# Kernel tuning notes

Measured on AMD Instinct MI355X. Metric: run time of the kernel, lower is better.

## Reference

```python
import jax, jax.numpy as jnp
import numpy as np

# ---- grid / solver constants (from opt) ----
NZ, NX = 300, 400
NPML, NPAD = 32, 0
NZP = NZ + 2 * NPML + NPAD   # 364 padded depth
NXP = NX + 2 * NPML          # 464 padded width
NSTEPS = 200
NSHOTS = 2
DX = 0.01    # km (moduli scaled by 1e-6 => velocities in km/s)
DT = 0.001   # s
SRC_Z = NPML + 2
REC_Z = NPML + 2


def _pad_model(m):
    # edge-replicate into the CPML halo + bottom pad, as ft.padding does
    return jnp.pad(m, ((NPML, NPML + NPAD), (NPML, NPML)), mode='edge')


def _sponge():
    # smooth absorbing profile in the nPml halo (sponge approximation of CPML)
    i = np.arange(NZP, dtype=np.float32)
    j = np.arange(NXP, dtype=np.float32)
    dz = np.clip(np.maximum(NPML - i, i - (NZP - 1 - NPML - NPAD)), 0, NPML) / NPML
    dx_ = np.clip(np.maximum(NPML - j, j - (NXP - 1 - NPML)), 0, NPML) / NPML
    d = dz[:, None] ** 2 + dx_[None, :] ** 2
    return jnp.asarray(np.exp(-0.1 * d), dtype=jnp.float32)


# staggered-grid finite differences (zero outside the grid)
def _dxf(f):
    return (jnp.pad(f[:, 1:], ((0, 0), (0, 1))) - f) / DX

def _dxb(f):
    return (f - jnp.pad(f[:, :-1], ((0, 0), (1, 0)))) / DX

def _dzf(f):
    return (jnp.pad(f[1:, :], ((0, 1), (0, 0))) - f) / DX

def _dzb(f):
    return (f - jnp.pad(f[:-1, :], ((1, 0), (0, 0)))) / DX


def _propagate(lam, mu, rho, stf, src_x, damp):
    """Elastic velocity-stress FDTD for one shot. stf: [NSTEPS]. Returns recs [NSTEPS, NX]."""
    lam2mu = lam + 2.0 * mu
    dt_rho = DT / rho
    zero = jnp.zeros((NZP, NXP), jnp.float32)

    def step(carry, s):
        vx, vz, sxx, szz, sxz = carry
        vx = (vx + dt_rho * (_dxf(sxx) + _dzb(sxz))) * damp
        vz = (vz + dt_rho * (_dxb(sxz) + _dzf(szz))) * damp
        dvx_dx = _dxb(vx)
        dvz_dz = _dzb(vz)
        sxx = (sxx + DT * (lam2mu * dvx_dx + lam * dvz_dz)) * damp
        szz = (szz + DT * (lam * dvx_dx + lam2mu * dvz_dz)) * damp
        sxz = (sxz + DT * mu * (_dzf(vx) + _dxf(vz))) * damp
        # explosive source injected into normal stresses
        sxx = sxx.at[SRC_Z, src_x].add(s * DT)
        szz = szz.at[SRC_Z, src_x].add(s * DT)
        rec = vx[REC_Z, NPML:NPML + NX]  # surface receiver line
        return (vx, vz, sxx, szz, sxz), rec

    init = (zero, zero, zero, zero, zero)
    _, recs = jax.lax.scan(step, init, stf)
    return recs


def _forward(Vp, Vs, Den, Stf, Mask, Shot_ids):
    Vp_pad = _pad_model(Vp)
    Vs_pad = _pad_model(Vs)
    Den_pad = _pad_model(Den)
    # masked models: gradient flows only where Mask == 1
    Vp_m = Mask * Vp_pad + (1.0 - Mask) * jax.lax.stop_gradient(Vp_pad)
    Vs_m = Mask * Vs_pad + (1.0 - Mask) * jax.lax.stop_gradient(Vs_pad)
    Den_m = Mask * Den_pad + (1.0 - Mask) * jax.lax.stop_gradient(Den_pad)
    Lam = (Vp_m ** 2 - 2.0 * Vs_m ** 2) * Den_m / 1.0e6
    Mu = Vs_m ** 2 * Den_m / 1.0e6

    damp = _sponge()
    ids = Shot_ids.astype(jnp.int32)
    src_x = NPML + 20 + ids * ((NX - 40) // NSHOTS)  # per-shot source x position
    stf = Stf[ids]                                   # [nshots, NSTEPS]
    recs = jax.vmap(lambda s, sx: _propagate(Lam, Mu, Den_m, s, sx, damp))(stf, src_x)
    return 0.5 * jnp.sum(recs.astype(jnp.float32) ** 2)  # scalar misfit


def setup_inputs() -> dict:
    key = jax.random.key(0)
    k1, k2 = jax.random.split(key)
    Vp = 2000.0 + 1500.0 * jax.random.uniform(k1, (NZ, NX), jnp.float32)   # m/s
    Vs = Vp / 1.732
    Den = 2000.0 + 500.0 * jax.random.uniform(k2, (NZ, NX), jnp.float32)   # kg/m^3
    # Ricker wavelet source, f0 = 10 Hz, shared across shots
    t = jnp.arange(NSTEPS, dtype=jnp.float32) * DT - 0.1
    f0 = 10.0
    arg = (jnp.pi * f0 * t) ** 2
    ricker = (1.0 - 2.0 * arg) * jnp.exp(-arg)
    Stf = jnp.broadcast_to(ricker, (NSHOTS, NSTEPS)).astype(jnp.float32)
    Mask = jnp.ones((NZP, NXP), jnp.float32)
    Shot_ids = jnp.arange(NSHOTS, dtype=jnp.int32)
    return {"Vp": Vp, "Vs": Vs, "Den": Den, "Stf": Stf, "Mask": Mask,
            "Shot_ids": Shot_ids, "ngpu": 1}


def reference(Vp, Vs, Den, Stf, Mask, Shot_ids, ngpu):
    return _forward(Vp, Vs, Den, Stf, Mask, Shot_ids)
```

## Files before the change

kernel.cpp:

```cpp
#include <hip/hip_runtime.h>
#include <cmath>

typedef unsigned long long u64;

namespace {
constexpr int kNZ = 300, kNX = 400;
constexpr int kNPML = 32;
constexpr int kNZP = 364, kNXP = 464;
constexpr int kNSTEPS = 200, kNSHOTS = 2;
constexpr int kSRC_Z = 34, kREC_Z = 34;
constexpr float kDT = 0.001f;
constexpr float kINV_DX = 100.0f;

constexpr int kR = 4;
constexpr int kNSLAB = 92;
constexpr int kNB = kNSLAB - 1;
constexpr int kBlocks = kNSHOTS * kNSLAB;
constexpr int kThreads = 512;
constexpr int kPitch = 468;
constexpr int kFStride = kR * kPitch;

constexpr int kFlagStride = 32;
constexpr int kHaloBase = 16384;
constexpr int kHaloCount = 2 * kNSHOTS * kNB * 2 * 6 * kNXP;
constexpr int kPartOff = kHaloBase + kHaloCount;
}

__global__ __launch_bounds__(kThreads, 1) void fwi_sim_kernel(
    const float* __restrict__ Vp, const float* __restrict__ Vs,
    const float* __restrict__ Den, const float* __restrict__ Stf,
    const int* __restrict__ Shot_ids, float* __restrict__ ws,
    float* __restrict__ out) {
    __shared__ float L[4 * kFStride];
    float* Lvx  = L;
    float* Lvz  = L + kFStride;
    float* Lsxx = L + 2 * kFStride;
    float* Lsxz = L + 3 * kFStride;

    const int blk  = blockIdx.x;
    const int s    = blk / kNSLAB;
    const int slab = blk - s * kNSLAB;
    const int r0   = slab * kR;
    const int tid  = threadIdx.x;
    const bool active = tid < kNXP;
    const int lc = tid + 1;

    int*   flags = (int*)ws;
    float* halo  = ws + kHaloBase;
    u64*   part  = (u64*)(ws + kPartOff);

    for (int q = tid; q < 4 * kFStride; q += kThreads) L[q] = 0.0f;

    auto modAt = [&](int i, int j, float& dtr_, float& dmp_, float& lam_,
                     float& mu_, float& l2m_) {
        dtr_ = dmp_ = lam_ = mu_ = l2m_ = 0.0f;
        if (i >= 0 && i < kNZP && j >= 0 && j < kNXP) {
            int iz = i - kNPML; iz = iz < 0 ? 0 : (iz > kNZ - 1 ? kNZ - 1 : iz);
            int jx = j - kNPML; jx = jx < 0 ? 0 : (jx > kNX - 1 ? kNX - 1 : jx);
            const float vp  = Vp[iz * kNX + jx];
            const float vs  = Vs[iz * kNX + jx];
            const float rho = Den[iz * kNX + jx];
            const float m = vs * vs * rho * 1e-6f;
            const float l = (vp * vp - 2.0f * vs * vs) * rho * 1e-6f;
            const float sc = kDT * kINV_DX;
            float dz = fmaxf((float)(kNPML - i), (float)(i - (kNZP - 1 - kNPML)));
            dz = fminf(fmaxf(dz, 0.0f), (float)kNPML) * (1.0f / kNPML);
            float dxx = fmaxf((float)(kNPML - j), (float)(j - (kNXP - 1 - kNPML)));
            dxx = fminf(fmaxf(dxx, 0.0f), (float)kNPML) * (1.0f / kNPML);
            dmp_ = expf(-0.1f * (dz * dz + dxx * dxx));
            dtr_ = kDT / rho * kINV_DX;
            lam_ = l * sc;
            mu_  = m * sc;
            l2m_ = (l + 2.0f * m) * sc;
        }
    };
    float rdtr[kR], rdamp[kR], rlam[kR], rmu[kR], rl2m[kR];
    float dtrT = 0, dmpT = 0, dtrB = 0, dmpB = 0;
    if (active) {
#pragma unroll
        for (int r = 0; r < kR; ++r)
            modAt(r0 + r, tid, rdtr[r], rdamp[r], rlam[r], rmu[r], rl2m[r]);
        float d0, d1, d2;
        modAt(r0 - 1, tid, dtrT, dmpT, d0, d1, d2);
        modAt(r0 + kR, tid, dtrB, dmpB, d0, d1, d2);
    }

    const int id  = Shot_ids[s];
    const int sxp = kNPML + 20 + id * ((kNX - 40) / kNSHOTS);
    const float* stf = Stf + id * kNSTEPS;
    const int rsrc = kSRC_Z - r0;
    const int rrec = kREC_Z - r0;
    const bool isRecBlock = (rrec >= 0 && rrec < kR);
    const float srcm = (active && tid == sxp) ? 1.0f : 0.0f;
    const float recm = (active && (unsigned)(tid - kNPML) < (unsigned)kNX) ? 1.0f : 0.0f;

    const bool hasTop = (slab > 0);
    const bool hasBot = (slab < kNSLAB - 1);
    int* ftopw = hasTop ? &flags[((s * kNB + (slab - 1)) * 2 + 1) * kFlagStride] : nullptr;
    int* fbotw = hasBot ? &flags[((s * kNB + slab) * 2 + 0) * kFlagStride] : nullptr;
    int* ftopr = hasTop ? &flags[((s * kNB + (slab - 1)) * 2 + 0) * kFlagStride] : nullptr;
    int* fbotr = hasBot ? &flags[((s * kNB + slab) * 2 + 1) * kFlagStride] : nullptr;
    auto hbase = [&](int buf, int b, int dir) {
        return halo + ((((buf * kNSHOTS + s) * kNB + b) * 2 + dir) * 6) * kNXP;
    };

    float fvx[kR]  = {}, fvz[kR]  = {}, fsxx[kR] = {}, fszz[kR] = {}, fsxz[kR] = {};
    float rsum = 0.0f;
    __syncthreads();

    for (int t = 0; t < kNSTEPS; ++t) {
        const int rb = (t & 1) ^ 1;
        const int wb = t & 1;

        if (active) {
#pragma unroll
            for (int r = 1; r <= kR - 2; ++r) {
                const float sxxC = fsxx[r];
                const float sxzC = fsxz[r];
                const float szzC = fszz[r];
                const float sxxR = Lsxx[r * kPitch + lc + 1];
                const float sxzL = Lsxz[r * kPitch + lc - 1];
                const float nvx = (fvx[r] + rdtr[r] * ((sxxR - sxxC) + (sxzC - fsxz[r - 1]))) * rdamp[r];
                const float nvz = (fvz[r] + rdtr[r] * ((sxzC - sxzL) + (fszz[r + 1] - szzC))) * rdamp[r];
                fvx[r] = nvx;
                fvz[r] = nvz;
                Lvx[r * kPitch + lc] = nvx;
                Lvz[r * kPitch + lc] = nvz;
                if (r == rrec) rsum += recm * nvx * nvx;
            }
        }

        if (t > 0) {
            if (hasTop) {
                while (__hip_atomic_load(ftopr, __ATOMIC_RELAXED, __HIP_MEMORY_SCOPE_AGENT) < t) {}
            }
            if (hasBot) {
                while (__hip_atomic_load(fbotr, __ATOMIC_RELAXED, __HIP_MEMORY_SCOPE_AGENT) < t) {}
            }
        }

        float h_vxT = 0, h_vzT = 0, h_sxxT = 0, h_szzT = 0, h_sxzT = 0, h_sxz2T = 0;
        float h_sxxT_r = 0, h_sxzT_l = 0;
        float h_vxB = 0, h_vzB = 0, h_sxxB = 0, h_sxzB = 0, h_szzB = 0, h_szz2B = 0;
        float h_sxxB_r = 0, h_sxzB_l = 0;
        if (t > 0 && active && hasTop) {
            const float* hb = hbase(rb, slab - 1, 0);
            h_vxT   = __hip_atomic_load(hb + tid,             __ATOMIC_RELAXED, __HIP_MEMORY_SCOPE_AGENT);
            h_vzT   = __hip_atomic_load(hb + kNXP + tid,      __ATOMIC_RELAXED, __HIP_MEMORY_SCOPE_AGENT);
            h_sxxT  = __hip_atomic_load(hb + 2 * kNXP + tid,  __ATOMIC_RELAXED, __HIP_MEMORY_SCOPE_AGENT);
            h_szzT  = __hip_atomic_load(hb + 3 * kNXP + tid,  __ATOMIC_RELAXED, __HIP_MEMORY_SCOPE_AGENT);
            h_sxzT  = __hip_atomic_load(hb + 4 * kNXP + tid,  __ATOMIC_RELAXED, __HIP_MEMORY_SCOPE_AGENT);
            h_sxz2T = __hip_atomic_load(hb + 5 * kNXP + tid,  __ATOMIC_RELAXED, __HIP_MEMORY_SCOPE_AGENT);
            if (tid < kNXP - 1) h_sxxT_r = __hip_atomic_load(hb + 2 * kNXP + tid + 1, __ATOMIC_RELAXED, __HIP_MEMORY_SCOPE_AGENT);
            if (tid > 0)        h_sxzT_l = __hip_atomic_load(hb + 4 * kNXP + tid - 1, __ATOMIC_RELAXED, __HIP_MEMORY_SCOPE_AGENT);
        }
        if (t > 0 && active && hasBot) {
            const float* hb = hbase(rb, slab, 1);
            h_vxB   = __hip_atomic_load(hb + tid,             __ATOMIC_RELAXED, __HIP_MEMORY_SCOPE_AGENT);
            h_vzB   = __hip_atomic_load(hb + kNXP + tid,      __ATOMIC_RELAXED, __HIP_MEMORY_SCOPE_AGENT);
            h_sxxB  = __hip_atomic_load(hb + 2 * kNXP + tid,  __ATOMIC_RELAXED, __HIP_MEMORY_SCOPE_AGENT);
            h_sxzB  = __hip_atomic_load(hb + 3 * kNXP + tid,  __ATOMIC_RELAXED, __HIP_MEMORY_SCOPE_AGENT);
            h_szzB  = __hip_atomic_load(hb + 4 * kNXP + tid,  __ATOMIC_RELAXED, __HIP_MEMORY_SCOPE_AGENT);
            h_szz2B = __hip_atomic_load(hb + 5 * kNXP + tid,  __ATOMIC_RELAXED, __HIP_MEMORY_SCOPE_AGENT);
            if (tid < kNXP - 1) h_sxxB_r = __hip_atomic_load(hb + 2 * kNXP + tid + 1, __ATOMIC_RELAXED, __HIP_MEMORY_SCOPE_AGENT);
            if (tid > 0)        h_sxzB_l = __hip_atomic_load(hb + 3 * kNXP + tid - 1, __ATOMIC_RELAXED, __HIP_MEMORY_SCOPE_AGENT);
        }

        float nvxT = 0, nvzT = 0, nvxB = 0, nvzB = 0;
        if (active) {
            nvxT = (h_vxT + dtrT * ((h_sxxT_r - h_sxxT) + (h_sxzT - h_sxz2T))) * dmpT;
            nvzT = (h_vzT + dtrT * ((h_sxzT - h_sxzT_l) + (fszz[0] - h_szzT))) * dmpT;
            nvxB = (h_vxB + dtrB * ((h_sxxB_r - h_sxxB) + (h_sxzB - fsxz[kR - 1]))) * dmpB;
            nvzB = (h_vzB + dtrB * ((h_sxzB - h_sxzB_l) + (h_szz2B - h_szzB))) * dmpB;
            {
                const float sxxC = fsxx[0], sxzC = fsxz[0], szzC = fszz[0];
                const float sxxR = Lsxx[lc + 1];
                const float sxzL = Lsxz[lc - 1];
                const float nvx = (fvx[0] + rdtr[0] * ((sxxR - sxxC) + (sxzC - h_sxzT))) * rdamp[0];
                const float nvz = (fvz[0] + rdtr[0] * ((sxzC - sxzL) + (fszz[1] - szzC))) * rdamp[0];
                fvx[0] = nvx; fvz[0] = nvz;
                Lvx[lc] = nvx; Lvz[lc] = nvz;
                if (0 == rrec) rsum += recm * nvx * nvx;
            }
            {
                const int r = kR - 1;
                const float sxxC = fsxx[r], sxzC = fsxz[r], szzC = fszz[r];
                const float sxxR = Lsxx[r * kPitch + lc + 1];
                const float sxzL = Lsxz[r * kPitch + lc - 1];
                const float nvx = (fvx[r] + rdtr[r] * ((sxxR - sxxC) + (sxzC - fsxz[r - 1]))) * rdamp[r];
                const float nvz = (fvz[r] + rdtr[r] * ((sxzC - sxzL) + (h_szzB - szzC))) * rdamp[r];
                fvx[r] = nvx; fvz[r] = nvz;
                Lvx[r * kPitch + lc] = nvx; Lvz[r * kPitch + lc] = nvz;
                if (r == rrec) rsum += recm * nvx * nvx;
            }
        }
        __syncthreads();

        if (active) {
            const float sval = stf[t] * kDT;
#pragma unroll
            for (int r = 0; r < kR; ++r) {
                const float vxC = fvx[r];
                const float vzC = fvz[r];
                const float vxL = Lvx[r * kPitch + lc - 1];
                const float vzR = Lvz[r * kPitch + lc + 1];
                const float vzU = (r > 0) ? fvz[r - 1] : nvzT;
                const float vxD = (r < kR - 1) ? fvx[r + 1] : nvxB;
                const float dvx = vxC - vxL;
                const float dvz = vzC - vzU;
                float nsxx = (fsxx[r] + (rl2m[r] * dvx + rlam[r] * dvz)) * rdamp[r];
                float nszz = (fszz[r] + (rlam[r] * dvx + rl2m[r] * dvz)) * rdamp[r];
                float nsxz = (fsxz[r] + rmu[r] * ((vxD - vxC) + (vzR - vzC))) * rdamp[r];
                if (r == rsrc) { nsxx += srcm * sval; nszz += srcm * sval; }
                fsxx[r] = nsxx;
                fszz[r] = nszz;
                fsxz[r] = nsxz;
                Lsxx[r * kPitch + lc] = nsxx;
                Lsxz[r * kPitch + lc] = nsxz;
            }
            if (hasTop) {
                float* hb = hbase(wb, slab - 1, 1);
                __hip_atomic_store(hb + tid,            fvx[0],  __ATOMIC_RELAXED, __HIP_MEMORY_SCOPE_AGENT);
                __hip_atomic_store(hb + kNXP + tid,     fvz[0],  __ATOMIC_RELAXED, __HIP_MEMORY_SCOPE_AGENT);
                __hip_atomic_store(hb + 2 * kNXP + tid, fsxx[0], __ATOMIC_RELAXED, __HIP_MEMORY_SCOPE_AGENT);
                __hip_atomic_store(hb + 3 * kNXP + tid, fsxz[0], __ATOMIC_RELAXED, __HIP_MEMORY_SCOPE_AGENT);
                __hip_atomic_store(hb + 4 * kNXP + tid, fszz[0], __ATOMIC_RELAXED, __HIP_MEMORY_SCOPE_AGENT);
                __hip_atomic_store(hb + 5 * kNXP + tid, fszz[1], __ATOMIC_RELAXED, __HIP_MEMORY_SCOPE_AGENT);
            }
            if (hasBot) {
                float* hb = hbase(wb, slab, 0);
                __hip_atomic_store(hb + tid,            fvx[kR - 1],  __ATOMIC_RELAXED, __HIP_MEMORY_SCOPE_AGENT);
                __hip_atomic_store(hb + kNXP + tid,     fvz[kR - 1],  __ATOMIC_RELAXED, __HIP_MEMORY_SCOPE_AGENT);
                __hip_atomic_store(hb + 2 * kNXP + tid, fsxx[kR - 1], __ATOMIC_RELAXED, __HIP_MEMORY_SCOPE_AGENT);
                __hip_atomic_store(hb + 3 * kNXP + tid, fszz[kR - 1], __ATOMIC_RELAXED, __HIP_MEMORY_SCOPE_AGENT);
                __hip_atomic_store(hb + 4 * kNXP + tid, fsxz[kR - 1], __ATOMIC_RELAXED, __HIP_MEMORY_SCOPE_AGENT);
                __hip_atomic_store(hb + 5 * kNXP + tid, fsxz[kR - 2], __ATOMIC_RELAXED, __HIP_MEMORY_SCOPE_AGENT);
            }
        }
        __syncthreads();
        if (tid == 0 && hasTop) __hip_atomic_store(ftopw, t + 1, __ATOMIC_RELAXED, __HIP_MEMORY_SCOPE_AGENT);
        if (tid == 1 && hasBot) __hip_atomic_store(fbotw, t + 1, __ATOMIC_RELAXED, __HIP_MEMORY_SCOPE_AGENT);
    }

    for (int off = 32; off > 0; off >>= 1) rsum += __shfl_down(rsum, off, 64);
    __syncthreads();
    if ((tid & 63) == 0) L[tid >> 6] = rsum;
    __syncthreads();
    if (isRecBlock && tid == 0) {
        float tot = 0.0f;
#pragma unroll
        for (int w = 0; w < kThreads / 64; ++w) tot += L[w];
        const u64 word = ((u64)1 << 32) | (u64)__float_as_uint(tot);
        __hip_atomic_store(&part[s], word, __ATOMIC_RELAXED, __HIP_MEMORY_SCOPE_AGENT);
    }
    if (blk == 0 && tid == 0) {
        u64 v0, v1;
        do { v0 = __hip_atomic_load(&part[0], __ATOMIC_RELAXED, __HIP_MEMORY_SCOPE_AGENT); }
        while ((int)(v0 >> 32) < 1);
        do { v1 = __hip_atomic_load(&part[1], __ATOMIC_RELAXED, __HIP_MEMORY_SCOPE_AGENT); }
        while ((int)(v1 >> 32) < 1);
        out[0] = 0.5f * (__uint_as_float((unsigned)v0) + __uint_as_float((unsigned)v1));
    }
}

extern "C" void kernel_launch(void* const* d_in, const int* in_sizes, int n_in,
                              void* d_out, int out_size, void* d_ws, size_t ws_size,
                              hipStream_t stream) {
    const float* Vp  = (const float*)d_in[0];
    const float* Vs  = (const float*)d_in[1];
    const float* Den = (const float*)d_in[2];
    const float* Stf = (const float*)d_in[3];
    const int* Shot_ids = (const int*)d_in[5];
    float* out = (float*)d_out;
    float* ws  = (float*)d_ws;

    fwi_sim_kernel<<<kBlocks, kThreads, 0, stream>>>(Vp, Vs, Den, Stf,
                                                     Shot_ids, ws, out);
}
```

Before: 604.8 us.

## Replace per-slab flag handshake with step-tagged 64-bit halo words

Each halo value is now stored as a 64-bit word that packs the step number with the float, so consumers poll the halo data directly instead of first spinning on a separate flag written after a block barrier. Halo loads are issued before the interior velocity update so their latency overlaps compute. The full __syncthreads calls are replaced by an LDS-only wait plus s_barrier, which drops the global-memory drain at each barrier. In exchange the halo traffic doubles in size, and correctness now relies on 64-bit atomic stores being seen whole and on the relaxed barrier still ordering the shared-memory accesses.

```diff
diff --git a/kernel.cpp b/kernel.cpp
--- a/kernel.cpp
+++ b/kernel.cpp
@@ -20,11 +20,20 @@
 constexpr int kPitch = 468;
 constexpr int kFStride = kR * kPitch;
 
-constexpr int kFlagStride = 32;
-constexpr int kHaloBase = 16384;
+constexpr int kHaloBaseB = 16384;
 constexpr int kHaloCount = 2 * kNSHOTS * kNB * 2 * 6 * kNXP;
-constexpr int kPartOff = kHaloBase + kHaloCount;
+constexpr size_t kPartOffB = kHaloBaseB + (size_t)kHaloCount * 8;
 }
+
+#define ALD(p)    __hip_atomic_load((p),       __ATOMIC_RELAXED, __HIP_MEMORY_SCOPE_AGENT)
+#define AST(p, v) __hip_atomic_store((p), (v), __ATOMIC_RELAXED, __HIP_MEMORY_SCOPE_AGENT)
+#define LDS_BAR() asm volatile("s_waitcnt lgkmcnt(0)\n\ts_barrier" ::: "memory")
+
+__device__ __forceinline__ u64 pk(int tag, float v) {
+    return ((u64)(unsigned)tag << 32) | (u64)__float_as_uint(v);
+}
+__device__ __forceinline__ float pf(u64 w) { return __uint_as_float((unsigned)w); }
+__device__ __forceinline__ int imn(int a, int b) { return a < b ? a : b; }
 
 __global__ __launch_bounds__(kThreads, 1) void fwi_sim_kernel(
     const float* __restrict__ Vp, const float* __restrict__ Vs,
@@ -45,9 +54,8 @@
     const bool active = tid < kNXP;
     const int lc = tid + 1;
 
-    int*   flags = (int*)ws;
-    float* halo  = ws + kHaloBase;
-    u64*   part  = (u64*)(ws + kPartOff);
+    u64* halo = (u64*)((char*)ws + kHaloBaseB);
+    u64* part = (u64*)((char*)ws + kPartOffB);
 
     for (int q = tid; q < 4 * kFStride; q += kThreads) L[q] = 0.0f;
 
@@ -96,13 +104,10 @@
 
     const bool hasTop = (slab > 0);
     const bool hasBot = (slab < kNSLAB - 1);
-    int* ftopw = hasTop ? &flags[((s * kNB + (slab - 1)) * 2 + 1) * kFlagStride] : nullptr;
-    int* fbotw = hasBot ? &flags[((s * kNB + slab) * 2 + 0) * kFlagStride] : nullptr;
-    int* ftopr = hasTop ? &flags[((s * kNB + (slab - 1)) * 2 + 0) * kFlagStride] : nullptr;
-    int* fbotr = hasBot ? &flags[((s * kNB + slab) * 2 + 1) * kFlagStride] : nullptr;
-    auto hbase = [&](int buf, int b, int dir) {
+    auto hbase = [&](int buf, int b, int dir) -> u64* {
         return halo + ((((buf * kNSHOTS + s) * kNB + b) * 2 + dir) * 6) * kNXP;
     };
+    const u64 kFresh = (u64)0x7fffffff << 32;
 
     float fvx[kR]  = {}, fvz[kR]  = {}, fsxx[kR] = {}, fszz[kR] = {}, fsxz[kR] = {};
     float rsum = 0.0f;
@@ -111,6 +116,33 @@
     for (int t = 0; t < kNSTEPS; ++t) {
         const int rb = (t & 1) ^ 1;
         const int wb = t & 1;
+        const bool doT = (t > 0) && active && hasTop;
+        const bool doB = (t > 0) && active && hasBot;
+        const u64* ht = hasTop ? hbase(rb, slab - 1, 0) : halo;
+        const u64* hbb = hasBot ? hbase(rb, slab, 1) : halo;
+
+        u64 wT0 = 0, wT1 = 0, wT2 = 0, wT3 = 0, wT4 = 0, wT5 = 0, wT6 = 0, wT7 = 0;
+        u64 wB0 = 0, wB1 = 0, wB2 = 0, wB3 = 0, wB4 = 0, wB5 = 0, wB6 = 0, wB7 = 0;
+        if (doT) {
+            wT0 = ALD(ht + tid);
+            wT1 = ALD(ht + kNXP + tid);
+            wT2 = ALD(ht + 2 * kNXP + tid);
+            wT3 = ALD(ht + 3 * kNXP + tid);
+            wT4 = ALD(ht + 4 * kNXP + tid);
+            wT5 = ALD(ht + 5 * kNXP + tid);
+            wT6 = (tid < kNXP - 1) ? ALD(ht + 2 * kNXP + tid + 1) : kFresh;
+            wT7 = (tid > 0)        ? ALD(ht + 4 * kNXP + tid - 1) : kFresh;
+        }
+        if (doB) {
+            wB0 = ALD(hbb + tid);
+            wB1 = ALD(hbb + kNXP + tid);
+            wB2 = ALD(hbb + 2 * kNXP + tid);
+            wB3 = ALD(hbb + 3 * kNXP + tid);
+            wB4 = ALD(hbb + 4 * kNXP + tid);
+            wB5 = ALD(hbb + 5 * kNXP + tid);
+            wB6 = (tid < kNXP - 1) ? ALD(hbb + 2 * kNXP + tid + 1) : kFresh;
+            wB7 = (tid > 0)        ? ALD(hbb + 3 * kNXP + tid - 1) : kFresh;
+        }
 
         if (active) {
 #pragma unroll
@@ -130,41 +162,49 @@
             }
         }
 
-        if (t > 0) {
-            if (hasTop) {
-                while (__hip_atomic_load(ftopr, __ATOMIC_RELAXED, __HIP_MEMORY_SCOPE_AGENT) < t) {}
-            }
-            if (hasBot) {
-                while (__hip_atomic_load(fbotr, __ATOMIC_RELAXED, __HIP_MEMORY_SCOPE_AGENT) < t) {}
-            }
-        }
-
-        float h_vxT = 0, h_vzT = 0, h_sxxT = 0, h_szzT = 0, h_sxzT = 0, h_sxz2T = 0;
-        float h_sxxT_r = 0, h_sxzT_l = 0;
-        float h_vxB = 0, h_vzB = 0, h_sxxB = 0, h_sxzB = 0, h_szzB = 0, h_szz2B = 0;
-        float h_sxxB_r = 0, h_sxzB_l = 0;
-        if (t > 0 && active && hasTop) {
-            const float* hb = hbase(rb, slab - 1, 0);
-            h_vxT   = __hip_atomic_load(hb + tid,             __ATOMIC_RELAXED, __HIP_MEMORY_SCOPE_AGENT);
-            h_vzT   = __hip_atomic_load(hb + kNXP + tid,      __ATOMIC_RELAXED, __HIP_MEMORY_SCOPE_AGENT);
-            h_sxxT  = __hip_atomic_load(hb + 2 * kNXP + tid,  __ATOMIC_RELAXED, __HIP_MEMORY_SCOPE_AGENT);
-            h_szzT  = __hip_atomic_load(hb + 3 * kNXP + tid,  __ATOMIC_RELAXED, __HIP_MEMORY_SCOPE_AGENT);
-            h_sxzT  = __hip_atomic_load(hb + 4 * kNXP + tid,  __ATOMIC_RELAXED, __HIP_MEMORY_SCOPE_AGENT);
-            h_sxz2T = __hip_atomic_load(hb + 5 * kNXP + tid,  __ATOMIC_RELAXED, __HIP_MEMORY_SCOPE_AGENT);
-            if (tid < kNXP - 1) h_sxxT_r = __hip_atomic_load(hb + 2 * kNXP + tid + 1, __ATOMIC_RELAXED, __HIP_MEMORY_SCOPE_AGENT);
-            if (tid > 0)        h_sxzT_l = __hip_atomic_load(hb + 4 * kNXP + tid - 1, __ATOMIC_RELAXED, __HIP_MEMORY_SCOPE_AGENT);
-        }
-        if (t > 0 && active && hasBot) {
-            const float* hb = hbase(rb, slab, 1);
-            h_vxB   = __hip_atomic_load(hb + tid,             __ATOMIC_RELAXED, __HIP_MEMORY_SCOPE_AGENT);
-            h_vzB   = __hip_atomic_load(hb + kNXP + tid,      __ATOMIC_RELAXED, __HIP_MEMORY_SCOPE_AGENT);
-            h_sxxB  = __hip_atomic_load(hb + 2 * kNXP + tid,  __ATOMIC_RELAXED, __HIP_MEMORY_SCOPE_AGENT);
-            h_sxzB  = __hip_atomic_load(hb + 3 * kNXP + tid,  __ATOMIC_RELAXED, __HIP_MEMORY_SCOPE_AGENT);
-            h_szzB  = __hip_atomic_load(hb + 4 * kNXP + tid,  __ATOMIC_RELAXED, __HIP_MEMORY_SCOPE_AGENT);
-            h_szz2B = __hip_atomic_load(hb + 5 * kNXP + tid,  __ATOMIC_RELAXED, __HIP_MEMORY_SCOPE_AGENT);
-            if (tid < kNXP - 1) h_sxxB_r = __hip_atomic_load(hb + 2 * kNXP + tid + 1, __ATOMIC_RELAXED, __HIP_MEMORY_SCOPE_AGENT);
-            if (tid > 0)        h_sxzB_l = __hip_atomic_load(hb + 3 * kNXP + tid - 1, __ATOMIC_RELAXED, __HIP_MEMORY_SCOPE_AGENT);
-        }
+        if (doT || doB) {
+            for (;;) {
+                int mn = 0x7fffffff;
+                if (doT) {
+                    mn = imn(mn, (int)(wT0 >> 32)); mn = imn(mn, (int)(wT1 >> 32));
+                    mn = imn(mn, (int)(wT2 >> 32)); mn = imn(mn, (int)(wT3 >> 32));
+                    mn = imn(mn, (int)(wT4 >> 32)); mn = imn(mn, (int)(wT5 >> 32));
+                    mn = imn(mn, (int)(wT6 >> 32)); mn = imn(mn, (int)(wT7 >> 32));
+                }
+                if (doB) {
+                    mn = imn(mn, (int)(wB0 >> 32)); mn = imn(mn, (int)(wB1 >> 32));
+                    mn = imn(mn, (int)(wB2 >> 32)); mn = imn(mn, (int)(wB3 >> 32));
+                    mn = imn(mn, (int)(wB4 >> 32)); mn = imn(mn, (int)(wB5 >> 32));
+                    mn = imn(mn, (int)(wB6 >> 32)); mn = imn(mn, (int)(wB7 >> 32));
+                }
+                if (mn >= t) break;
+                if (doT) {
+                    wT0 = ALD(ht + tid);
+                    wT1 = ALD(ht + kNXP + tid);
+                    wT2 = ALD(ht + 2 * kNXP + tid);
+                    wT3 = ALD(ht + 3 * kNXP + tid);
+                    wT4 = ALD(ht + 4 * kNXP + tid);
+                    wT5 = ALD(ht + 5 * kNXP + tid);
+                    wT6 = (tid < kNXP - 1) ? ALD(ht + 2 * kNXP + tid + 1) : kFresh;
+                    wT7 = (tid > 0)        ? ALD(ht + 4 * kNXP + tid - 1) : kFresh;
+                }
+                if (doB) {
+                    wB0 = ALD(hbb + tid);
+                    wB1 = ALD(hbb + kNXP + tid);
+                    wB2 = ALD(hbb + 2 * kNXP + tid);
+                    wB3 = ALD(hbb + 3 * kNXP + tid);
+                    wB4 = ALD(hbb + 4 * kNXP + tid);
+                    wB5 = ALD(hbb + 5 * kNXP + tid);
+                    wB6 = (tid < kNXP - 1) ? ALD(hbb + 2 * kNXP + tid + 1) : kFresh;
+                    wB7 = (tid > 0)        ? ALD(hbb + 3 * kNXP + tid - 1) : kFresh;
+                }
+            }
+        }
+
+        const float h_vxT = pf(wT0), h_vzT = pf(wT1), h_sxxT = pf(wT2), h_szzT = pf(wT3);
+        const float h_sxzT = pf(wT4), h_sxz2T = pf(wT5), h_sxxT_r = pf(wT6), h_sxzT_l = pf(wT7);
+        const float h_vxB = pf(wB0), h_vzB = pf(wB1), h_sxxB = pf(wB2), h_sxzB = pf(wB3);
+        const float h_szzB = pf(wB4), h_szz2B = pf(wB5), h_sxxB_r = pf(wB6), h_sxzB_l = pf(wB7);
 
         float nvxT = 0, nvzT = 0, nvxB = 0, nvzB = 0;
         if (active) {
@@ -194,7 +234,7 @@
                 if (r == rrec) rsum += recm * nvx * nvx;
             }
         }
-        __syncthreads();
+        LDS_BAR();
 
         if (active) {
             const float sval = stf[t] * kDT;
@@ -218,28 +258,27 @@
                 Lsxx[r * kPitch + lc] = nsxx;
                 Lsxz[r * kPitch + lc] = nsxz;
             }
+            const int tg = t + 1;
             if (hasTop) {
-                float* hb = hbase(wb, slab - 1, 1);
-                __hip_atomic_store(hb + tid,            fvx[0],  __ATOMIC_RELAXED, __HIP_MEMORY_SCOPE_AGENT);
-                __hip_atomic_store(hb + kNXP + tid,     fvz[0],  __ATOMIC_RELAXED, __HIP_MEMORY_SCOPE_AGENT);
-                __hip_atomic_store(hb + 2 * kNXP + tid, fsxx[0], __ATOMIC_RELAXED, __HIP_MEMORY_SCOPE_AGENT);
-                __hip_atomic_store(hb + 3 * kNXP + tid, fsxz[0], __ATOMIC_RELAXED, __HIP_MEMORY_SCOPE_AGENT);
-                __hip_atomic_store(hb + 4 * kNXP + tid, fszz[0], __ATOMIC_RELAXED, __HIP_MEMORY_SCOPE_AGENT);
-                __hip_atomic_store(hb + 5 * kNXP + tid, fszz[1], __ATOMIC_RELAXED, __HIP_MEMORY_SCOPE_AGENT);
+                u64* hp = hbase(wb, slab - 1, 1);
+                AST(hp + tid,            pk(tg, fvx[0]));
+                AST(hp + kNXP + tid,     pk(tg, fvz[0]));
+                AST(hp + 2 * kNXP + tid, pk(tg, fsxx[0]));
+                AST(hp + 3 * kNXP + tid, pk(tg, fsxz[0]));
+                AST(hp + 4 * kNXP + tid, pk(tg, fszz[0]));
+                AST(hp + 5 * kNXP + tid, pk(tg, fszz[1]));
             }
             if (hasBot) {
-                float* hb = hbase(wb, slab, 0);
-                __hip_atomic_store(hb + tid,            fvx[kR - 1],  __ATOMIC_RELAXED, __HIP_MEMORY_SCOPE_AGENT);
-                __hip_atomic_store(hb + kNXP + tid,     fvz[kR - 1],  __ATOMIC_RELAXED, __HIP_MEMORY_SCOPE_AGENT);
-                __hip_atomic_store(hb + 2 * kNXP + tid, fsxx[kR - 1], __ATOMIC_RELAXED, __HIP_MEMORY_SCOPE_AGENT);
-                __hip_atomic_store(hb + 3 * kNXP + tid, fszz[kR - 1], __ATOMIC_RELAXED, __HIP_MEMORY_SCOPE_AGENT);
-                __hip_atomic_store(hb + 4 * kNXP + tid, fsxz[kR - 1], __ATOMIC_RELAXED, __HIP_MEMORY_SCOPE_AGENT);
-                __hip_atomic_store(hb + 5 * kNXP + tid, fsxz[kR - 2], __ATOMIC_RELAXED, __HIP_MEMORY_SCOPE_AGENT);
-            }
-        }
-        __syncthreads();
-        if (tid == 0 && hasTop) __hip_atomic_store(ftopw, t + 1, __ATOMIC_RELAXED, __HIP_MEMORY_SCOPE_AGENT);
-        if (tid == 1 && hasBot) __hip_atomic_store(fbotw, t + 1, __ATOMIC_RELAXED, __HIP_MEMORY_SCOPE_AGENT);
+                u64* hp = hbase(wb, slab, 0);
+                AST(hp + tid,            pk(tg, fvx[kR - 1]));
+                AST(hp + kNXP + tid,     pk(tg, fvz[kR - 1]));
+                AST(hp + 2 * kNXP + tid, pk(tg, fsxx[kR - 1]));
+                AST(hp + 3 * kNXP + tid, pk(tg, fszz[kR - 1]));
+                AST(hp + 4 * kNXP + tid, pk(tg, fsxz[kR - 1]));
+                AST(hp + 5 * kNXP + tid, pk(tg, fsxz[kR - 2]));
+            }
+        }
+        LDS_BAR();
     }
 
     for (int off = 32; off > 0; off >>= 1) rsum += __shfl_down(rsum, off, 64);
@@ -251,14 +290,12 @@
 #pragma unroll
         for (int w = 0; w < kThreads / 64; ++w) tot += L[w];
         const u64 word = ((u64)1 << 32) | (u64)__float_as_uint(tot);
-        __hip_atomic_store(&part[s], word, __ATOMIC_RELAXED, __HIP_MEMORY_SCOPE_AGENT);
+        AST(&part[s], word);
     }
     if (blk == 0 && tid == 0) {
         u64 v0, v1;
-        do { v0 = __hip_atomic_load(&part[0], __ATOMIC_RELAXED, __HIP_MEMORY_SCOPE_AGENT); }
-        while ((int)(v0 >> 32) < 1);
-        do { v1 = __hip_atomic_load(&part[1], __ATOMIC_RELAXED, __HIP_MEMORY_SCOPE_AGENT); }
-        while ((int)(v1 >> 32) < 1);
+        do { v0 = ALD(&part[0]); } while ((int)(v0 >> 32) < 1);
+        do { v1 = ALD(&part[1]); } while ((int)(v1 >> 32) < 1);
         out[0] = 0.5f * (__uint_as_float((unsigned)v0) + __uint_as_float((unsigned)v1));
     }
 }
```

Result: slower. 995.8 us (+64.7%).

## Exchange ghost-zone halos every two timesteps with redundant overlap computation

Applied to the files above, without the earlier changes.

Each slab now keeps a 12-row window (4 owned rows plus 4 ghost rows per side) and advances two timesteps per inter-block handshake. Halo exchange sends 16 planes per neighbour once per chunk instead of 6 planes per step, and ghost rows are recomputed redundantly to shrink the trapezoid. The goal is to halve the number of global spin-wait synchronisations, which dominate this latency-bound kernel. In exchange there is extra redundant arithmetic and register use, single-buffered halo slots that need new ack flags, and replacing __syncthreads with inline-asm barriers.

```diff
diff --git a/kernel.cpp b/kernel.cpp
--- a/kernel.cpp
+++ b/kernel.cpp
@@ -13,29 +13,69 @@
 constexpr float kINV_DX = 100.0f;
 
 constexpr int kR = 4;
+constexpr int kG = 4;
+constexpr int kW = 12;
 constexpr int kNSLAB = 92;
 constexpr int kNB = kNSLAB - 1;
 constexpr int kBlocks = kNSHOTS * kNSLAB;
 constexpr int kThreads = 512;
 constexpr int kPitch = 468;
-constexpr int kFStride = kR * kPitch;
+constexpr int kChunks = kNSTEPS / 2;
 
 constexpr int kFlagStride = 32;
 constexpr int kHaloBase = 16384;
-constexpr int kHaloCount = 2 * kNSHOTS * kNB * 2 * 6 * kNXP;
+constexpr int kSlots = 16;
+constexpr int kHaloCount = kNSHOTS * kNB * 2 * kSlots * kNXP;
 constexpr int kPartOff = kHaloBase + kHaloCount;
 }
+
+#define ALD(p)    __hip_atomic_load((p),       __ATOMIC_RELAXED, __HIP_MEMORY_SCOPE_AGENT)
+#define AST(p, v) __hip_atomic_store((p), (v), __ATOMIC_RELAXED, __HIP_MEMORY_SCOPE_AGENT)
+#define LDS_BAR() asm volatile("s_waitcnt lgkmcnt(0)\n\ts_barrier" ::: "memory")
+
+#define VEL_ROWS(ELO, EHI)                                                     \
+  if (active) {                                                                \
+    _Pragma("unroll")                                                          \
+    for (int e = (ELO); e <= (EHI); ++e) {                                     \
+      const float sxxC = fsxx[e], sxzC = fsxz[e], szzC = fszz[e];              \
+      const float sxxR = Lsxx[e * kPitch + lc + 1];                            \
+      const float sxzL = Lsxz[e * kPitch + lc - 1];                            \
+      const float nvx = (fvx[e] + rdtr[e] * ((sxxR - sxxC) + (sxzC - fsxz[e - 1]))) * rdamp[e]; \
+      const float nvz = (fvz[e] + rdtr[e] * ((sxzC - sxzL) + (fszz[e + 1] - szzC))) * rdamp[e]; \
+      fvx[e] = nvx; fvz[e] = nvz;                                              \
+      Lvx[e * kPitch + lc] = nvx; Lvz[e * kPitch + lc] = nvz;                  \
+      if (e == erec) rsum += recm * nvx * nvx;                                 \
+    }                                                                          \
+  }
+
+#define STRESS_ROWS(ELO, EHI, SVAL)                                            \
+  if (active) {                                                                \
+    _Pragma("unroll")                                                          \
+    for (int e = (ELO); e <= (EHI); ++e) {                                     \
+      const float vxC = fvx[e], vzC = fvz[e];                                  \
+      const float vxL = Lvx[e * kPitch + lc - 1];                              \
+      const float vzR = Lvz[e * kPitch + lc + 1];                              \
+      const float dvx = vxC - vxL;                                             \
+      const float dvz = vzC - fvz[e - 1];                                      \
+      float nsxx = (fsxx[e] + (rl2m[e] * dvx + rlam[e] * dvz)) * rdamp[e];     \
+      float nszz = (fszz[e] + (rlam[e] * dvx + rl2m[e] * dvz)) * rdamp[e];     \
+      float nsxz = (fsxz[e] + rmu[e] * ((fvx[e + 1] - vxC) + (vzR - vzC))) * rdamp[e]; \
+      if (e == ersrc) { nsxx += srcm * (SVAL); nszz += srcm * (SVAL); }        \
+      fsxx[e] = nsxx; fszz[e] = nszz; fsxz[e] = nsxz;                          \
+      Lsxx[e * kPitch + lc] = nsxx; Lsxz[e * kPitch + lc] = nsxz;              \
+    }                                                                          \
+  }
 
 __global__ __launch_bounds__(kThreads, 1) void fwi_sim_kernel(
     const float* __restrict__ Vp, const float* __restrict__ Vs,
     const float* __restrict__ Den, const float* __restrict__ Stf,
     const int* __restrict__ Shot_ids, float* __restrict__ ws,
     float* __restrict__ out) {
-    __shared__ float L[4 * kFStride];
+    __shared__ float L[4 * kW * kPitch];
     float* Lvx  = L;
-    float* Lvz  = L + kFStride;
-    float* Lsxx = L + 2 * kFStride;
-    float* Lsxz = L + 3 * kFStride;
+    float* Lvz  = L + kW * kPitch;
+    float* Lsxx = L + 2 * kW * kPitch;
+    float* Lsxz = L + 3 * kW * kPitch;
 
     const int blk  = blockIdx.x;
     const int s    = blk / kNSLAB;
@@ -49,7 +89,7 @@
     float* halo  = ws + kHaloBase;
     u64*   part  = (u64*)(ws + kPartOff);
 
-    for (int q = tid; q < 4 * kFStride; q += kThreads) L[q] = 0.0f;
+    for (int q = tid; q < 4 * kW * kPitch; q += kThreads) L[q] = 0.0f;
 
     auto modAt = [&](int i, int j, float& dtr_, float& dmp_, float& lam_,
                      float& mu_, float& l2m_) {
@@ -74,23 +114,21 @@
             l2m_ = (l + 2.0f * m) * sc;
         }
     };
-    float rdtr[kR], rdamp[kR], rlam[kR], rmu[kR], rl2m[kR];
-    float dtrT = 0, dmpT = 0, dtrB = 0, dmpB = 0;
+    float rdtr[kW], rdamp[kW], rlam[kW], rmu[kW], rl2m[kW];
     if (active) {
 #pragma unroll
-        for (int r = 0; r < kR; ++r)
-            modAt(r0 + r, tid, rdtr[r], rdamp[r], rlam[r], rmu[r], rl2m[r]);
-        float d0, d1, d2;
-        modAt(r0 - 1, tid, dtrT, dmpT, d0, d1, d2);
-        modAt(r0 + kR, tid, dtrB, dmpB, d0, d1, d2);
+        for (int e = 0; e < kW; ++e)
+            modAt(r0 + e - kG, tid, rdtr[e], rdamp[e], rlam[e], rmu[e], rl2m[e]);
     }
 
     const int id  = Shot_ids[s];
     const int sxp = kNPML + 20 + id * ((kNX - 40) / kNSHOTS);
     const float* stf = Stf + id * kNSTEPS;
-    const int rsrc = kSRC_Z - r0;
-    const int rrec = kREC_Z - r0;
-    const bool isRecBlock = (rrec >= 0 && rrec < kR);
+    int ersrc = kSRC_Z - r0 + kG;
+    if (ersrc < 0 || ersrc >= kW) ersrc = -1;
+    int erec = kREC_Z - r0 + kG;
+    if (erec < kG || erec >= kG + kR) erec = -1;
+    const bool isRecBlock = (erec >= 0);
     const float srcm = (active && tid == sxp) ? 1.0f : 0.0f;
     const float recm = (active && (unsigned)(tid - kNPML) < (unsigned)kNX) ? 1.0f : 0.0f;
 
@@ -100,146 +138,141 @@
     int* fbotw = hasBot ? &flags[((s * kNB + slab) * 2 + 0) * kFlagStride] : nullptr;
     int* ftopr = hasTop ? &flags[((s * kNB + (slab - 1)) * 2 + 0) * kFlagStride] : nullptr;
     int* fbotr = hasBot ? &flags[((s * kNB + slab) * 2 + 1) * kFlagStride] : nullptr;
-    auto hbase = [&](int buf, int b, int dir) {
-        return halo + ((((buf * kNSHOTS + s) * kNB + b) * 2 + dir) * 6) * kNXP;
+    int* acktw = hasTop ? ftopr + 16 : nullptr;
+    int* ackbw = hasBot ? fbotr + 16 : nullptr;
+    int* ackbr = hasBot ? fbotw + 16 : nullptr;
+    int* acktr = hasTop ? ftopw + 16 : nullptr;
+    auto hslot = [&](int b, int dir) -> float* {
+        return halo + (size_t)(((s * kNB + b) * 2 + dir) * kSlots) * kNXP;
     };
 
-    float fvx[kR]  = {}, fvz[kR]  = {}, fsxx[kR] = {}, fszz[kR] = {}, fsxz[kR] = {};
+    float fvx[kW]  = {}, fvz[kW]  = {}, fsxx[kW] = {}, fszz[kW] = {}, fsxz[kW] = {};
     float rsum = 0.0f;
     __syncthreads();
 
-    for (int t = 0; t < kNSTEPS; ++t) {
-        const int rb = (t & 1) ^ 1;
-        const int wb = t & 1;
-
-        if (active) {
-#pragma unroll
-            for (int r = 1; r <= kR - 2; ++r) {
-                const float sxxC = fsxx[r];
-                const float sxzC = fsxz[r];
-                const float szzC = fszz[r];
-                const float sxxR = Lsxx[r * kPitch + lc + 1];
-                const float sxzL = Lsxz[r * kPitch + lc - 1];
-                const float nvx = (fvx[r] + rdtr[r] * ((sxxR - sxxC) + (sxzC - fsxz[r - 1]))) * rdamp[r];
-                const float nvz = (fvz[r] + rdtr[r] * ((sxzC - sxzL) + (fszz[r + 1] - szzC))) * rdamp[r];
-                fvx[r] = nvx;
-                fvz[r] = nvz;
-                Lvx[r * kPitch + lc] = nvx;
-                Lvz[r * kPitch + lc] = nvz;
-                if (r == rrec) rsum += recm * nvx * nvx;
+    for (int c = 0; c < kChunks; ++c) {
+        const float sval0 = stf[2 * c] * kDT;
+        const float sval1 = stf[2 * c + 1] * kDT;
+
+        VEL_ROWS(5, 6)
+
+        if (c > 0) {
+            if (hasTop) { while (ALD(ftopr) < c) {} }
+            if (hasBot) { while (ALD(fbotr) < c) {} }
+            if (active && hasTop) {
+                const float* hb = hslot(slab - 1, 0);
+                fvx[1]  = ALD(hb +  0 * kNXP + tid);
+                fvx[2]  = ALD(hb +  1 * kNXP + tid);
+                fvx[3]  = ALD(hb +  2 * kNXP + tid);
+                fvz[1]  = ALD(hb +  3 * kNXP + tid);
+                fvz[2]  = ALD(hb +  4 * kNXP + tid);
+                fvz[3]  = ALD(hb +  5 * kNXP + tid);
+                fsxx[1] = ALD(hb +  6 * kNXP + tid);
+                fsxx[2] = ALD(hb +  7 * kNXP + tid);
+                fsxx[3] = ALD(hb +  8 * kNXP + tid);
+                fszz[1] = ALD(hb +  9 * kNXP + tid);
+                fszz[2] = ALD(hb + 10 * kNXP + tid);
+                fszz[3] = ALD(hb + 11 * kNXP + tid);
+                fsxz[0] = ALD(hb + 12 * kNXP + tid);
+                fsxz[1] = ALD(hb + 13 * kNXP + tid);
+                fsxz[2] = ALD(hb + 14 * kNXP + tid);
+                fsxz[3] = ALD(hb + 15 * kNXP + tid);
             }
-        }
-
-        if (t > 0) {
-            if (hasTop) {
-                while (__hip_atomic_load(ftopr, __ATOMIC_RELAXED, __HIP_MEMORY_SCOPE_AGENT) < t) {}
+            if (active && hasBot) {
+                const float* hb = hslot(slab, 1);
+                fvx[8]   = ALD(hb +  0 * kNXP + tid);
+                fvx[9]   = ALD(hb +  1 * kNXP + tid);
+                fvx[10]  = ALD(hb +  2 * kNXP + tid);
+                fvz[8]   = ALD(hb +  3 * kNXP + tid);
+                fvz[9]   = ALD(hb +  4 * kNXP + tid);
+                fvz[10]  = ALD(hb +  5 * kNXP + tid);
+                fsxx[8]  = ALD(hb +  6 * kNXP + tid);
+                fsxx[9]  = ALD(hb +  7 * kNXP + tid);
+                fsxx[10] = ALD(hb +  8 * kNXP + tid);
+                fsxz[8]  = ALD(hb +  9 * kNXP + tid);
+                fsxz[9]  = ALD(hb + 10 * kNXP + tid);
+                fsxz[10] = ALD(hb + 11 * kNXP + tid);
+                fszz[8]  = ALD(hb + 12 * kNXP + tid);
+                fszz[9]  = ALD(hb + 13 * kNXP + tid);
+                fszz[10] = ALD(hb + 14 * kNXP + tid);
+                fszz[11] = ALD(hb + 15 * kNXP + tid);
             }
-            if (hasBot) {
-                while (__hip_atomic_load(fbotr, __ATOMIC_RELAXED, __HIP_MEMORY_SCOPE_AGENT) < t) {}
+            asm volatile("s_waitcnt vmcnt(0)" ::: "memory");
+            if (active && hasTop) {
+                Lsxx[1 * kPitch + lc] = fsxx[1];
+                Lsxx[2 * kPitch + lc] = fsxx[2];
+                Lsxx[3 * kPitch + lc] = fsxx[3];
+                Lsxz[1 * kPitch + lc] = fsxz[1];
+                Lsxz[2 * kPitch + lc] = fsxz[2];
+                Lsxz[3 * kPitch + lc] = fsxz[3];
             }
-        }
-
-        float h_vxT = 0, h_vzT = 0, h_sxxT = 0, h_szzT = 0, h_sxzT = 0, h_sxz2T = 0;
-        float h_sxxT_r = 0, h_sxzT_l = 0;
-        float h_vxB = 0, h_vzB = 0, h_sxxB = 0, h_sxzB = 0, h_szzB = 0, h_szz2B = 0;
-        float h_sxxB_r = 0, h_sxzB_l = 0;
-        if (t > 0 && active && hasTop) {
-            const float* hb = hbase(rb, slab - 1, 0);
-            h_vxT   = __hip_atomic_load(hb + tid,             __ATOMIC_RELAXED, __HIP_MEMORY_SCOPE_AGENT);
-            h_vzT   = __hip_atomic_load(hb + kNXP + tid,      __ATOMIC_RELAXED, __HIP_MEMORY_SCOPE_AGENT);
-            h_sxxT  = __hip_atomic_load(hb + 2 * kNXP + tid,  __ATOMIC_RELAXED, __HIP_MEMORY_SCOPE_AGENT);
-            h_szzT  = __hip_atomic_load(hb + 3 * kNXP + tid,  __ATOMIC_RELAXED, __HIP_MEMORY_SCOPE_AGENT);
-            h_sxzT  = __hip_atomic_load(hb + 4 * kNXP + tid,  __ATOMIC_RELAXED, __HIP_MEMORY_SCOPE_AGENT);
-            h_sxz2T = __hip_atomic_load(hb + 5 * kNXP + tid,  __ATOMIC_RELAXED, __HIP_MEMORY_SCOPE_AGENT);
-            if (tid < kNXP - 1) h_sxxT_r = __hip_atomic_load(hb + 2 * kNXP + tid + 1, __ATOMIC_RELAXED, __HIP_MEMORY_SCOPE_AGENT);
-            if (tid > 0)        h_sxzT_l = __hip_atomic_load(hb + 4 * kNXP + tid - 1, __ATOMIC_RELAXED, __HIP_MEMORY_SCOPE_AGENT);
-        }
-        if (t > 0 && active && hasBot) {
-            const float* hb = hbase(rb, slab, 1);
-            h_vxB   = __hip_atomic_load(hb + tid,             __ATOMIC_RELAXED, __HIP_MEMORY_SCOPE_AGENT);
-            h_vzB   = __hip_atomic_load(hb + kNXP + tid,      __ATOMIC_RELAXED, __HIP_MEMORY_SCOPE_AGENT);
-            h_sxxB  = __hip_atomic_load(hb + 2 * kNXP + tid,  __ATOMIC_RELAXED, __HIP_MEMORY_SCOPE_AGENT);
-            h_sxzB  = __hip_atomic_load(hb + 3 * kNXP + tid,  __ATOMIC_RELAXED, __HIP_MEMORY_SCOPE_AGENT);
-            h_szzB  = __hip_atomic_load(hb + 4 * kNXP + tid,  __ATOMIC_RELAXED, __HIP_MEMORY_SCOPE_AGENT);
-            h_szz2B = __hip_atomic_load(hb + 5 * kNXP + tid,  __ATOMIC_RELAXED, __HIP_MEMORY_SCOPE_AGENT);
-            if (tid < kNXP - 1) h_sxxB_r = __hip_atomic_load(hb + 2 * kNXP + tid + 1, __ATOMIC_RELAXED, __HIP_MEMORY_SCOPE_AGENT);
-            if (tid > 0)        h_sxzB_l = __hip_atomic_load(hb + 3 * kNXP + tid - 1, __ATOMIC_RELAXED, __HIP_MEMORY_SCOPE_AGENT);
-        }
-
-        float nvxT = 0, nvzT = 0, nvxB = 0, nvzB = 0;
-        if (active) {
-            nvxT = (h_vxT + dtrT * ((h_sxxT_r - h_sxxT) + (h_sxzT - h_sxz2T))) * dmpT;
-            nvzT = (h_vzT + dtrT * ((h_sxzT - h_sxzT_l) + (fszz[0] - h_szzT))) * dmpT;
-            nvxB = (h_vxB + dtrB * ((h_sxxB_r - h_sxxB) + (h_sxzB - fsxz[kR - 1]))) * dmpB;
-            nvzB = (h_vzB + dtrB * ((h_sxzB - h_sxzB_l) + (h_szz2B - h_szzB))) * dmpB;
-            {
-                const float sxxC = fsxx[0], sxzC = fsxz[0], szzC = fszz[0];
-                const float sxxR = Lsxx[lc + 1];
-                const float sxzL = Lsxz[lc - 1];
-                const float nvx = (fvx[0] + rdtr[0] * ((sxxR - sxxC) + (sxzC - h_sxzT))) * rdamp[0];
-                const float nvz = (fvz[0] + rdtr[0] * ((sxzC - sxzL) + (fszz[1] - szzC))) * rdamp[0];
-                fvx[0] = nvx; fvz[0] = nvz;
-                Lvx[lc] = nvx; Lvz[lc] = nvz;
-                if (0 == rrec) rsum += recm * nvx * nvx;
+            if (active && hasBot) {
+                Lsxx[8 * kPitch + lc]  = fsxx[8];
+                Lsxx[9 * kPitch + lc]  = fsxx[9];
+                Lsxx[10 * kPitch + lc] = fsxx[10];
+                Lsxz[8 * kPitch + lc]  = fsxz[8];
+                Lsxz[9 * kPitch + lc]  = fsxz[9];
+                Lsxz[10 * kPitch + lc] = fsxz[10];
             }
-            {
-                const int r = kR - 1;
-                const float sxxC = fsxx[r], sxzC = fsxz[r], szzC = fszz[r];
-                const float sxxR = Lsxx[r * kPitch + lc + 1];
-                const float sxzL = Lsxz[r * kPitch + lc - 1];
-                const float nvx = (fvx[r] + rdtr[r] * ((sxxR - sxxC) + (sxzC - fsxz[r - 1]))) * rdamp[r];
-                const float nvz = (fvz[r] + rdtr[r] * ((sxzC - sxzL) + (h_szzB - szzC))) * rdamp[r];
-                fvx[r] = nvx; fvz[r] = nvz;
-                Lvx[r * kPitch + lc] = nvx; Lvz[r * kPitch + lc] = nvz;
-                if (r == rrec) rsum += recm * nvx * nvx;
-            }
+            LDS_BAR();
+            if (tid == 0 && hasTop) AST(acktw, c);
+            if (tid == 1 && hasBot) AST(ackbw, c);
+        }
+
+        VEL_ROWS(1, 4)
+        VEL_ROWS(7, 10)
+        LDS_BAR();
+        STRESS_ROWS(2, 9, sval0)
+        LDS_BAR();
+        VEL_ROWS(3, 8)
+        LDS_BAR();
+        STRESS_ROWS(4, 7, sval1)
+
+        if (c > 0) {
+            if (hasBot) { while (ALD(ackbr) < c) {} }
+            if (hasTop) { while (ALD(acktr) < c) {} }
+        }
+        if (active && hasBot) {
+            float* hb = hslot(slab, 0);
+            AST(hb +  0 * kNXP + tid, fvx[5]);
+            AST(hb +  1 * kNXP + tid, fvx[6]);
+            AST(hb +  2 * kNXP + tid, fvx[7]);
+            AST(hb +  3 * kNXP + tid, fvz[5]);
+            AST(hb +  4 * kNXP + tid, fvz[6]);
+            AST(hb +  5 * kNXP + tid, fvz[7]);
+            AST(hb +  6 * kNXP + tid, fsxx[5]);
+            AST(hb +  7 * kNXP + tid, fsxx[6]);
+            AST(hb +  8 * kNXP + tid, fsxx[7]);
+            AST(hb +  9 * kNXP + tid, fszz[5]);
+            AST(hb + 10 * kNXP + tid, fszz[6]);
+            AST(hb + 11 * kNXP + tid, fszz[7]);
+            AST(hb + 12 * kNXP + tid, fsxz[4]);
+            AST(hb + 13 * kNXP + tid, fsxz[5]);
+            AST(hb + 14 * kNXP + tid, fsxz[6]);
+            AST(hb + 15 * kNXP + tid, fsxz[7]);
+        }
+        if (active && hasTop) {
+            float* hb = hslot(slab - 1, 1);
+            AST(hb +  0 * kNXP + tid, fvx[4]);
+            AST(hb +  1 * kNXP + tid, fvx[5]);
+            AST(hb +  2 * kNXP + tid, fvx[6]);
+            AST(hb +  3 * kNXP + tid, fvz[4]);
+            AST(hb +  4 * kNXP + tid, fvz[5]);
+            AST(hb +  5 * kNXP + tid, fvz[6]);
+            AST(hb +  6 * kNXP + tid, fsxx[4]);
+            AST(hb +  7 * kNXP + tid, fsxx[5]);
+            AST(hb +  8 * kNXP + tid, fsxx[6]);
+            AST(hb +  9 * kNXP + tid, fsxz[4]);
+            AST(hb + 10 * kNXP + tid, fsxz[5]);
+            AST(hb + 11 * kNXP + tid, fsxz[6]);
+            AST(hb + 12 * kNXP + tid, fszz[4]);
+            AST(hb + 13 * kNXP + tid, fszz[5]);
+            AST(hb + 14 * kNXP + tid, fszz[6]);
+            AST(hb + 15 * kNXP + tid, fszz[7]);
         }
         __syncthreads();
-
-        if (active) {
-            const float sval = stf[t] * kDT;
-#pragma unroll
-            for (int r = 0; r < kR; ++r) {
-                const float vxC = fvx[r];
-                const float vzC = fvz[r];
-                const float vxL = Lvx[r * kPitch + lc - 1];
-                const float vzR = Lvz[r * kPitch + lc + 1];
-                const float vzU = (r > 0) ? fvz[r - 1] : nvzT;
-                const float vxD = (r < kR - 1) ? fvx[r + 1] : nvxB;
-                const float dvx = vxC - vxL;
-                const float dvz = vzC - vzU;
-                float nsxx = (fsxx[r] + (rl2m[r] * dvx + rlam[r] * dvz)) * rdamp[r];
-                float nszz = (fszz[r] + (rlam[r] * dvx + rl2m[r] * dvz)) * rdamp[r];
-                float nsxz = (fsxz[r] + rmu[r] * ((vxD - vxC) + (vzR - vzC))) * rdamp[r];
-                if (r == rsrc) { nsxx += srcm * sval; nszz += srcm * sval; }
-                fsxx[r] = nsxx;
-                fszz[r] = nszz;
-                fsxz[r] = nsxz;
-                Lsxx[r * kPitch + lc] = nsxx;
-                Lsxz[r * kPitch + lc] = nsxz;
-            }
-            if (hasTop) {
-                float* hb = hbase(wb, slab - 1, 1);
-                __hip_atomic_store(hb + tid,            fvx[0],  __ATOMIC_RELAXED, __HIP_MEMORY_SCOPE_AGENT);
-                __hip_atomic_store(hb + kNXP + tid,     fvz[0],  __ATOMIC_RELAXED, __HIP_MEMORY_SCOPE_AGENT);
-                __hip_atomic_store(hb + 2 * kNXP + tid, fsxx[0], __ATOMIC_RELAXED, __HIP_MEMORY_SCOPE_AGENT);
-                __hip_atomic_store(hb + 3 * kNXP + tid, fsxz[0], __ATOMIC_RELAXED, __HIP_MEMORY_SCOPE_AGENT);
-                __hip_atomic_store(hb + 4 * kNXP + tid, fszz[0], __ATOMIC_RELAXED, __HIP_MEMORY_SCOPE_AGENT);
-                __hip_atomic_store(hb + 5 * kNXP + tid, fszz[1], __ATOMIC_RELAXED, __HIP_MEMORY_SCOPE_AGENT);
-            }
-            if (hasBot) {
-                float* hb = hbase(wb, slab, 0);
-                __hip_atomic_store(hb + tid,            fvx[kR - 1],  __ATOMIC_RELAXED, __HIP_MEMORY_SCOPE_AGENT);
-                __hip_atomic_store(hb + kNXP + tid,     fvz[kR - 1],  __ATOMIC_RELAXED, __HIP_MEMORY_SCOPE_AGENT);
-                __hip_atomic_store(hb + 2 * kNXP + tid, fsxx[kR - 1], __ATOMIC_RELAXED, __HIP_MEMORY_SCOPE_AGENT);
-                __hip_atomic_store(hb + 3 * kNXP + tid, fszz[kR - 1], __ATOMIC_RELAXED, __HIP_MEMORY_SCOPE_AGENT);
-                __hip_atomic_store(hb + 4 * kNXP + tid, fsxz[kR - 1], __ATOMIC_RELAXED, __HIP_MEMORY_SCOPE_AGENT);
-                __hip_atomic_store(hb + 5 * kNXP + tid, fsxz[kR - 2], __ATOMIC_RELAXED, __HIP_MEMORY_SCOPE_AGENT);
-            }
-        }
-        __syncthreads();
-        if (tid == 0 && hasTop) __hip_atomic_store(ftopw, t + 1, __ATOMIC_RELAXED, __HIP_MEMORY_SCOPE_AGENT);
-        if (tid == 1 && hasBot) __hip_atomic_store(fbotw, t + 1, __ATOMIC_RELAXED, __HIP_MEMORY_SCOPE_AGENT);
+        if (tid == 0 && hasTop) AST(ftopw, c + 1);
+        if (tid == 1 && hasBot) AST(fbotw, c + 1);
     }
 
     for (int off = 32; off > 0; off >>= 1) rsum += __shfl_down(rsum, off, 64);
@@ -251,14 +284,12 @@
 #pragma unroll
         for (int w = 0; w < kThreads / 64; ++w) tot += L[w];
         const u64 word = ((u64)1 << 32) | (u64)__float_as_uint(tot);
-        __hip_atomic_store(&part[s], word, __ATOMIC_RELAXED, __HIP_MEMORY_SCOPE_AGENT);
+        AST(&part[s], word);
     }
     if (blk == 0 && tid == 0) {
         u64 v0, v1;
-        do { v0 = __hip_atomic_load(&part[0], __ATOMIC_RELAXED, __HIP_MEMORY_SCOPE_AGENT); }
-        while ((int)(v0 >> 32) < 1);
-        do { v1 = __hip_atomic_load(&part[1], __ATOMIC_RELAXED, __HIP_MEMORY_SCOPE_AGENT); }
-        while ((int)(v1 >> 32) < 1);
+        do { v0 = ALD(&part[0]); } while ((int)(v0 >> 32) < 1);
+        do { v1 = ALD(&part[1]); } while ((int)(v1 >> 32) < 1);
         out[0] = 0.5f * (__uint_as_float((unsigned)v0) + __uint_as_float((unsigned)v1));
     }
 }
```

Measured after the change: 1.407 ms. 2.33x slower.
